# Performance work log

Hardware: AMD Instinct MI355X
Metric: run time of the kernel (lower is better)

The kernel has to match this reference:

```python
import jax, jax.numpy as jnp
import numpy as np

MAX_LENGTH = 41
SOS_index = 0


def setup_inputs() -> dict:
    key = jax.random.key(0)
    ks = jax.random.split(key, 16)
    B, S, H, V = 32, 41, 1024, 16384
    sc = 0.02
    inp = {
        "encoder_outputs": jax.random.normal(ks[0], (B, S, H), jnp.float32),
        "encoder_hidden": jax.random.normal(ks[1], (1, B, H), jnp.float32),
        "target_tensor": jax.random.randint(ks[2], (B, MAX_LENGTH), 0, V, jnp.int64),
        # embedding table
        "emb": jax.random.normal(ks[3], (V, H), jnp.float32) * sc,
        # Bahdanau attention params
        "Wq": jax.random.normal(ks[4], (H, H), jnp.float32) * sc,
        "bq": jnp.zeros((H,), jnp.float32),
        "Wk": jax.random.normal(ks[5], (H, H), jnp.float32) * sc,
        "bk": jnp.zeros((H,), jnp.float32),
        "Vw": jax.random.normal(ks[6], (1, H), jnp.float32) * sc,
        "bV": jnp.zeros((1,), jnp.float32),
        # LSTM params (PyTorch gate order: i, f, g, o)
        "Wih": jax.random.normal(ks[7], (4 * H, 2 * H), jnp.float32) * sc,
        "Whh": jax.random.normal(ks[8], (4 * H, H), jnp.float32) * sc,
        "bih": jnp.zeros((4 * H,), jnp.float32),
        "bhh": jnp.zeros((4 * H,), jnp.float32),
        # output projection
        "Wout": jax.random.normal(ks[9], (V, H), jnp.float32) * sc,
        "bout": jnp.zeros((V,), jnp.float32),
    }
    return inp


def reference(encoder_outputs, encoder_hidden, target_tensor, emb,
              Wq, bq, Wk, bk, Vw, bV, Wih, Whh, bih, bhh, Wout, bout):
    B = encoder_outputs.shape[0]
    H = encoder_outputs.shape[2]
    # keys projection is invariant across decode steps
    keys_proj = jnp.einsum('bsh,gh->bsg', encoder_outputs, Wk) + bk  # [B,S,H]
    # teacher-forced input tokens: SOS then target[:, :-1]
    sos = jnp.full((1, B), SOS_index, dtype=target_tensor.dtype)
    tokens = jnp.concatenate([sos, target_tensor.T[:-1]], axis=0)  # [T,B]

    h0 = encoder_hidden[0]            # [B,H]
    c0 = jnp.zeros_like(h0)

    def step(carry, tok):
        h, c = carry
        x = emb[tok]                                       # [B,H] (dropout: eval mode)
        q = h @ Wq.T + bq                                  # [B,H] query from hidden
        e = jnp.tanh(q[:, None, :] + keys_proj)            # [B,S,H]
        scores = jnp.einsum('bsh,h->bs', e, Vw[0]) + bV[0] # [B,S]
        w = jax.nn.softmax(scores, axis=-1)                # [B,S]
        ctx = jnp.einsum('bs,bsh->bh', w, encoder_outputs) # [B,H]
        xi = jnp.concatenate([x, ctx], axis=-1)            # [B,2H]
        gates = xi @ Wih.T + h @ Whh.T + (bih + bhh)       # [B,4H]
        i_g, f_g, g_g, o_g = jnp.split(gates, 4, axis=-1)
        i_g = jax.nn.sigmoid(i_g)
        f_g = jax.nn.sigmoid(f_g)
        g_g = jnp.tanh(g_g)
        o_g = jax.nn.sigmoid(o_g)
        c_new = f_g * c + i_g * g_g
        h_new = o_g * jnp.tanh(c_new)
        logits = h_new @ Wout.T + bout                     # [B,V]
        return (h_new, c_new), (logits, w)

    (h_f, c_f), (logits, attn) = jax.lax.scan(step, (h0, c0), tokens)
    decoder_outputs = jax.nn.log_softmax(logits.transpose(1, 0, 2), axis=-1)  # [B,T,V]
    attentions = attn.transpose(1, 0, 2)                                       # [B,T,S]
    return decoder_outputs, h_f[None], c_f[None], attentions
```

## Files before the change

### kernel.cpp

```cpp
#include <hip/hip_runtime.h>
#include <hip/hip_bf16.h>
#include <math.h>

#define B 32
#define S 41
#define T 41
#define H 1024
#define V 16384
#define BH (B*H)
#define NBLK 256
#define NTHR 512
#define RPB 20

typedef unsigned int uint;
typedef unsigned short ushort;
typedef __attribute__((ext_vector_type(8))) short bf16x8;
typedef __attribute__((ext_vector_type(4))) float f32x4;
typedef _Float16 h2v __attribute__((ext_vector_type(2)));

__device__ __forceinline__ float fast_sigmoid(float x){ return 1.f/(1.f + __expf(-x)); }
__device__ __forceinline__ float fast_tanh(float x){
  float e = __expf(-2.f*fabsf(x));
  float r = (1.f - e)/(1.f + e);
  return copysignf(r, x);
}
__device__ __forceinline__ ushort f2h(float f){ return __builtin_bit_cast(unsigned short, (_Float16)f); }
__device__ __forceinline__ float h2f(ushort u){ return (float)__builtin_bit_cast(_Float16, u); }
__device__ __forceinline__ h2v bc2(uint u){ return __builtin_bit_cast(h2v, u); }
__device__ __forceinline__ ushort f2bf(float f){
  uint u = __float_as_uint(f);
  u = u + 0x7FFFu + ((u>>16)&1u);
  return (ushort)(u>>16);
}

#if defined(__has_builtin)
#if __has_builtin(__builtin_amdgcn_fdot2)
#define HAS_FDOT2 1
#endif
#endif
__device__ __forceinline__ float dot2(h2v a, h2v b, float c){
#ifdef HAS_FDOT2
  return __builtin_amdgcn_fdot2(a, b, c, false);
#else
  return fmaf((float)a.x, (float)b.x, fmaf((float)a.y, (float)b.y, c));
#endif
}

__device__ __forceinline__ void st_sc_f32(float* p, float v){
  asm volatile("global_store_dword %0, %1, off sc0 sc1" :: "v"(p), "v"(v) : "memory");
}
__device__ __forceinline__ void st_sc_u32(uint* p, uint v){
  asm volatile("global_store_dword %0, %1, off sc0 sc1" :: "v"(p), "v"(v) : "memory");
}

__device__ __forceinline__ float ld_sc_f32(const float* p){
  float r;
  asm volatile("global_load_dword %0, %1, off sc0 sc1\n\ts_waitcnt vmcnt(0)"
               : "=v"(r) : "v"(p) : "memory");
  return r;
}
__device__ __forceinline__ void ldx8_sc(const uint* p, uint4* r){
  asm volatile(
    "global_load_dwordx4 %0, %8, off sc0 sc1\n\t"
    "global_load_dwordx4 %1, %8, off offset:16 sc0 sc1\n\t"
    "global_load_dwordx4 %2, %8, off offset:32 sc0 sc1\n\t"
    "global_load_dwordx4 %3, %8, off offset:48 sc0 sc1\n\t"
    "global_load_dwordx4 %4, %8, off offset:64 sc0 sc1\n\t"
    "global_load_dwordx4 %5, %8, off offset:80 sc0 sc1\n\t"
    "global_load_dwordx4 %6, %8, off offset:96 sc0 sc1\n\t"
    "global_load_dwordx4 %7, %8, off offset:112 sc0 sc1\n\t"
    "s_waitcnt vmcnt(0)"
    : "=&v"(r[0]), "=&v"(r[1]), "=&v"(r[2]), "=&v"(r[3]),
      "=&v"(r[4]), "=&v"(r[5]), "=&v"(r[6]), "=&v"(r[7])
    : "v"(p) : "memory");
}
__device__ __forceinline__ void ld_qgh_sc(const float* qp, const float* gp,
                                          float4* q, float* gh){
  asm volatile(
    "global_load_dwordx4 %0, %5, off sc0 sc1\n\t"
    "global_load_dwordx4 %1, %5, off offset:16 sc0 sc1\n\t"
    "global_load_dwordx4 %2, %5, off offset:32 sc0 sc1\n\t"
    "global_load_dwordx4 %3, %5, off offset:48 sc0 sc1\n\t"
    "global_load_dword  %4, %6, off sc0 sc1\n\t"
    "s_waitcnt vmcnt(0)"
    : "=&v"(q[0]), "=&v"(q[1]), "=&v"(q[2]), "=&v"(q[3]), "=&v"(*gh)
    : "v"(qp), "v"(gp) : "memory");
}

__device__ __forceinline__ void gbar_flat(uint* cnt, uint target){
  asm volatile("s_waitcnt vmcnt(0)" ::: "memory");
  __syncthreads();
  if (threadIdx.x == 0){
    __hip_atomic_fetch_add(cnt, 1u, __ATOMIC_RELAXED, __HIP_MEMORY_SCOPE_AGENT);
    while (__hip_atomic_load(cnt, __ATOMIC_RELAXED, __HIP_MEMORY_SCOPE_AGENT) < target)
      __builtin_amdgcn_s_sleep(1);
  }
  __syncthreads();
}

__global__ __launch_bounds__(256) void k_init(const float* __restrict__ eh,
                                              ushort* __restrict__ h16, uint* __restrict__ bar){
  int i = blockIdx.x*256 + threadIdx.x;
  h16[i] = f2h(eh[i]);
  if (i < 1024) bar[i] = 0;
}

__global__ __launch_bounds__(256) void k_bsum(const float* __restrict__ a,
                                              const float* __restrict__ b, float* __restrict__ o){
  int i = blockIdx.x*256 + threadIdx.x;
  o[i] = a[i] + b[i];
}

__global__ __launch_bounds__(256) void k_gather(const float* __restrict__ emb,
    const int* __restrict__ tgt, float* __restrict__ Xall){
  int r = blockIdx.x;
  int t = r / B, b = r % B;
  int tok = (t==0) ? 0 : tgt[b*T + (t-1)];
  const float4* src = (const float4*)(emb + (size_t)tok*H);
  float4* dst = (float4*)(Xall + (size_t)r*H);
  dst[threadIdx.x] = src[threadIdx.x];
}

__global__ __launch_bounds__(256) void k_cvt16(const float* __restrict__ src,
                                               ushort* __restrict__ dst, int n8){
  int i = blockIdx.x*256 + threadIdx.x;
  if (i >= n8) return;
  const float4* s4 = (const float4*)src + (size_t)i*2;
  float4 a = s4[0], b = s4[1];
  union { ushort us[8]; uint4 v; } p;
  p.us[0]=f2h(a.x); p.us[1]=f2h(a.y); p.us[2]=f2h(a.z); p.us[3]=f2h(a.w);
  p.us[4]=f2h(b.x); p.us[5]=f2h(b.y); p.us[6]=f2h(b.z); p.us[7]=f2h(b.w);
  ((uint4*)dst)[i] = p.v;
}

__global__ __launch_bounds__(256) void k_bgemm(const float* __restrict__ A,
    const float* __restrict__ W, const float* __restrict__ bias, float* __restrict__ C,
    int M, int N, int wstride, int woff)
{
  __shared__ ushort As[128*40];
  __shared__ ushort Bs[128*40];
  const int tid = threadIdx.x;
  const int n0 = blockIdx.x*128, m0 = blockIdx.y*128;
  const int row = tid>>1, half = tid&1;
  const int lane = tid & 63, widx = tid >> 6;
  const int wm = (widx>>1)*64, wn = (widx&1)*64;

  int arow = m0 + row; if (arow > M-1) arow = M-1;
  const float* ga = A + (size_t)arow*1024 + half*16;
  const float* gw = W + (size_t)(n0+row)*wstride + woff + half*16;
  ushort* sa = &As[row*40 + half*16];
  ushort* sb = &Bs[row*40 + half*16];

  f32x4 acc[4][4] = {};

  for (int k0 = 0; k0 < 1024; k0 += 32) {
    float4 a0 = *(const float4*)(ga+k0),   a1 = *(const float4*)(ga+k0+4);
    float4 a2 = *(const float4*)(ga+k0+8), a3 = *(const float4*)(ga+k0+12);
    float4 w0 = *(const float4*)(gw+k0),   w1 = *(const float4*)(gw+k0+4);
    float4 w2 = *(const float4*)(gw+k0+8), w3 = *(const float4*)(gw+k0+12);
    __syncthreads();
    {
      union { ushort us[8]; uint4 v; } p, q;
      p.us[0]=f2bf(a0.x); p.us[1]=f2bf(a0.y); p.us[2]=f2bf(a0.z); p.us[3]=f2bf(a0.w);
      p.us[4]=f2bf(a1.x); p.us[5]=f2bf(a1.y); p.us[6]=f2bf(a1.z); p.us[7]=f2bf(a1.w);
      q.us[0]=f2bf(a2.x); q.us[1]=f2bf(a2.y); q.us[2]=f2bf(a2.z); q.us[3]=f2bf(a2.w);
      q.us[4]=f2bf(a3.x); q.us[5]=f2bf(a3.y); q.us[6]=f2bf(a3.z); q.us[7]=f2bf(a3.w);
      *(uint4*)sa = p.v; *(uint4*)(sa+8) = q.v;
      p.us[0]=f2bf(w0.x); p.us[1]=f2bf(w0.y); p.us[2]=f2bf(w0.z); p.us[3]=f2bf(w0.w);
      p.us[4]=f2bf(w1.x); p.us[5]=f2bf(w1.y); p.us[6]=f2bf(w1.z); p.us[7]=f2bf(w1.w);
      q.us[0]=f2bf(w2.x); q.us[1]=f2bf(w2.y); q.us[2]=f2bf(w2.z); q.us[3]=f2bf(w2.w);
      q.us[4]=f2bf(w3.x); q.us[5]=f2bf(w3.y); q.us[6]=f2bf(w3.z); q.us[7]=f2bf(w3.w);
      *(uint4*)sb = p.v; *(uint4*)(sb+8) = q.v;
    }
    __syncthreads();
    bf16x8 af[4], bf[4];
    #pragma unroll
    for (int i=0;i<4;i++)
      af[i] = *(const bf16x8*)&As[(wm + i*16 + (lane&15))*40 + (lane>>4)*8];
    #pragma unroll
    for (int j=0;j<4;j++)
      bf[j] = *(const bf16x8*)&Bs[(wn + j*16 + (lane&15))*40 + (lane>>4)*8];
    #pragma unroll
    for (int i=0;i<4;i++)
      #pragma unroll
      for (int j=0;j<4;j++)
        acc[i][j] = __builtin_amdgcn_mfma_f32_16x16x32_bf16(af[i], bf[j], acc[i][j], 0, 0, 0);
  }

  #pragma unroll
  for (int i=0;i<4;i++){
    #pragma unroll
    for (int j=0;j<4;j++){
      int n = n0 + wn + j*16 + (lane&15);
      float bv = bias ? bias[n] : 0.f;
      #pragma unroll
      for (int qq=0;qq<4;qq++){
        int m = m0 + wm + i*16 + ((lane>>4)<<2) + qq;
        if (m < M) C[(size_t)m*N + n] = acc[i][j][qq] + bv;
      }
    }
  }
}

__global__ __launch_bounds__(512, 2) void k_loop(
    const ushort* __restrict__ Wc16,
    const float* __restrict__ bq,
    const ushort* __restrict__ keys16,
    const float* __restrict__ Vw, const float* __restrict__ bV,
    const float* __restrict__ GxF,
    const ushort* __restrict__ encW16,
    float* __restrict__ qg,
    float* __restrict__ ghg,
    ushort* __restrict__ h16,
    float* __restrict__ hhist,
    float* __restrict__ attn_out,
    float* __restrict__ hf, float* __restrict__ cf,
    uint* __restrict__ bar,
    float* __restrict__ pscore)
{
  __shared__ __align__(16) uint   w_lds[RPB*516];
  __shared__ __align__(16) ushort ew_lds[512*42];
  __shared__ __align__(16) float  red[RPB*512];
  __shared__ float sc_sh[64];
  __shared__ float ga[512];
  __shared__ float hsh[128];

  const int tid = threadIdx.x;
  const int bid = blockIdx.x;
  const int pb_b = bid >> 3, pb_mc = bid & 7;
  const int lane = tid & 63, wv = tid >> 6;
  uint* h16u = (uint*)h16;

  const int pa_b = tid & 31, pa_ks = tid >> 5;
  const int gn = (tid >> 7)*H + pb_mc*128 + (tid & 127);

  const int na = bid*RPB + (tid>>5);
  const int nb = bid*RPB + 16 + (tid>>5);
  const float bqa = (na < H) ? bq[na] : 0.f;
  const float bqb = (tid < 128 && nb < H) ? bq[nb] : 0.f;

  uint* qcnt = &bar[0];
  uint* hcnt = &bar[16];
  uint* scnt = &bar[256 + pb_b*8];
  const int my_s = pb_mc + 8*wv;

  for (int i = tid; i < RPB*128; i += NTHR){
    int r = i >> 7, j = i & 127;
    uint4 v = *((const uint4*)(Wc16 + (size_t)(bid*RPB + r)*1024) + j);
    *(uint4*)&w_lds[r*516 + j*4] = v;
  }
  for (int s = 0; s < S; ++s)
    ew_lds[tid*42 + s] = encW16[((size_t)pb_b*S + s)*4096 + gn];
  float vreg[16];
  {
    const float4* vp = (const float4*)(Vw + lane*16);
    *(float4*)&vreg[0] = vp[0]; *(float4*)&vreg[4]  = vp[1];
    *(float4*)&vreg[8] = vp[2]; *(float4*)&vreg[12] = vp[3];
  }
  const float bV0 = bV[0];
  float creg = 0.f;
  __syncthreads();

  for (int t = 0; t < T; ++t) {
    float gxv;
    {
      uint4 hr[8];
      ldx8_sc((const uint*)h16u + pa_b*512 + pa_ks*32, hr);
      float part[RPB];
      #pragma unroll
      for (int r = 0; r < RPB; ++r){
        const uint* wr = &w_lds[r*516 + pa_ks*32];
        float a0 = 0.f, a1 = 0.f;
        #pragma unroll
        for (int j = 0; j < 8; ++j){
          uint4 w = *(const uint4*)(wr + j*4);
          uint4 h = hr[j];
          a0 = dot2(bc2(w.x), bc2(h.x), a0);
          a1 = dot2(bc2(w.y), bc2(h.y), a1);
          a0 = dot2(bc2(w.z), bc2(h.z), a0);
          a1 = dot2(bc2(w.w), bc2(h.w), a1);
        }
        part[r] = a0 + a1;
      }
      #pragma unroll
      for (int r = 0; r < RPB; ++r) red[r*512 + pa_ks*32 + pa_b] = part[r];
      __syncthreads();
      {
        int r = tid >> 5, b2 = tid & 31;
        const float* rp = &red[r*512 + b2];
        float s = 0.f;
        #pragma unroll
        for (int k2 = 0; k2 < 16; ++k2) s += rp[k2*32];
        if (na < H) st_sc_f32(&qg[b2*H + na], s + bqa);
        else        st_sc_f32(&ghg[(size_t)b2*4*H + (na - H)], s);
      }
      if (tid < 128){
        int r = 16 + (tid >> 5), b2 = tid & 31;
        const float* rp = &red[r*512 + b2];
        float s = 0.f;
        #pragma unroll
        for (int k2 = 0; k2 < 16; ++k2) s += rp[k2*32];
        if (nb < H) st_sc_f32(&qg[b2*H + nb], s + bqb);
        else        st_sc_f32(&ghg[(size_t)b2*4*H + (nb - H)], s);
      }
      gxv = GxF[((size_t)t*B + pb_b)*4*H + gn];
    }
    gbar_flat(qcnt, 256u*(uint)(t+1));

    {
      float4 q4[4]; float ghv;
      ld_qgh_sc(qg + pb_b*H + lane*16, ghg + (size_t)pb_b*4*H + gn, q4, &ghv);
      float qarr[16];
      *(float4*)&qarr[0] = q4[0]; *(float4*)&qarr[4]  = q4[1];
      *(float4*)&qarr[8] = q4[2]; *(float4*)&qarr[12] = q4[3];

      if (my_s < S) {
        const ushort* kr = keys16 + ((size_t)pb_b*S + my_s)*H + lane*16;
        uint4 k0 = *(const uint4*)kr;
        uint4 k1 = *(const uint4*)(kr + 8);
        float part = 0.f;
        #define SC2(u, e) { h2v hh = bc2(u); \
          part += fast_tanh(qarr[e]   + (float)hh.x) * vreg[e]; \
          part += fast_tanh(qarr[e+1] + (float)hh.y) * vreg[e+1]; }
        SC2(k0.x,0) SC2(k0.y,2) SC2(k0.z,4) SC2(k0.w,6)
        SC2(k1.x,8) SC2(k1.y,10) SC2(k1.z,12) SC2(k1.w,14)
        #undef SC2
        #pragma unroll
        for (int off = 32; off > 0; off >>= 1) part += __shfl_xor(part, off);
        if (lane == 0) st_sc_f32(&pscore[pb_b*64 + my_s], part + bV0);
      }
      asm volatile("s_waitcnt vmcnt(0)" ::: "memory");
      __syncthreads();
      if (tid == 0){
        __hip_atomic_fetch_add(scnt, 1u, __ATOMIC_RELAXED, __HIP_MEMORY_SCOPE_AGENT);
        while (__hip_atomic_load(scnt, __ATOMIC_RELAXED, __HIP_MEMORY_SCOPE_AGENT) < 8u*(uint)(t+1))
          __builtin_amdgcn_s_sleep(1);
      }
      __syncthreads();
      if (tid < 64) {
        float val = (tid < S) ? ld_sc_f32(&pscore[pb_b*64 + tid]) : -1e30f;
        float m = val;
        #pragma unroll
        for (int off = 32; off > 0; off >>= 1) m = fmaxf(m, __shfl_xor(m, off));
        float e = (tid < S) ? __expf(val - m) : 0.f;
        float ssum = e;
        #pragma unroll
        for (int off = 32; off > 0; off >>= 1) ssum += __shfl_xor(ssum, off);
        if (tid < S) {
          float w = e / ssum;
          sc_sh[tid] = w;
          if (pb_mc == 0) attn_out[((size_t)pb_b*T + t)*S + tid] = w;
        }
      }
      __syncthreads();
      {
        float acc = gxv + ghv;
        const ushort* ep = &ew_lds[tid*42];
        #pragma unroll
        for (int s = 0; s < S; ++s)
          acc = fmaf(sc_sh[s], h2f(ep[s]), acc);
        ga[tid] = acc;
      }
      __syncthreads();
      if (tid < 128) {
        float ig = fast_sigmoid(ga[tid]);
        float fg = fast_sigmoid(ga[128+tid]);
        float gg = fast_tanh   (ga[256+tid]);
        float og = fast_sigmoid(ga[384+tid]);
        creg = fg*creg + ig*gg;
        float hn = og * fast_tanh(creg);
        int m = pb_mc*128 + tid;
        hsh[tid] = hn;
        __builtin_nontemporal_store(hn, &hhist[((size_t)pb_b*T + t)*H + m]);
        if (t == T-1) { hf[pb_b*H + m] = hn; cf[pb_b*H + m] = creg; }
      }
      __syncthreads();
      if (tid < 64) {
        uint pk = (uint)f2h(hsh[2*tid]) | ((uint)f2h(hsh[2*tid+1]) << 16);
        st_sc_u32(&h16u[(size_t)pb_b*512 + pb_mc*64 + tid], pk);
      }
    }
    if (t < T-1) gbar_flat(hcnt, 256u*(uint)(t+1));
  }
}

__global__ __launch_bounds__(256) void k_logsm(float* __restrict__ p_all)
{
  float* p = p_all + (size_t)blockIdx.x * V;
  const int tid = threadIdx.x;
  const int lane = tid & 63, wave = tid >> 6;
  __shared__ float red[4];
  float4 v[16];
  float m = -1e30f;
  #pragma unroll
  for (int j=0;j<16;j++){
    v[j] = *(const float4*)(p + 4*(tid + 256*j));
    m = fmaxf(m, fmaxf(fmaxf(v[j].x, v[j].y), fmaxf(v[j].z, v[j].w)));
  }
  #pragma unroll
  for (int off=32; off>0; off>>=1) m = fmaxf(m, __shfl_xor(m, off));
  if (lane==0) red[wave] = m;
  __syncthreads();
  m = fmaxf(fmaxf(red[0], red[1]), fmaxf(red[2], red[3]));
  float ssum = 0.f;
  #pragma unroll
  for (int j=0;j<16;j++){
    ssum += __expf(v[j].x - m) + __expf(v[j].y - m) + __expf(v[j].z - m) + __expf(v[j].w - m);
  }
  #pragma unroll
  for (int off=32; off>0; off>>=1) ssum += __shfl_xor(ssum, off);
  __syncthreads();
  if (lane==0) red[wave] = ssum;
  __syncthreads();
  float lse = m + __logf(red[0] + red[1] + red[2] + red[3]);
  #pragma unroll
  for (int j=0;j<16;j++){
    float4 o; o.x = v[j].x - lse; o.y = v[j].y - lse; o.z = v[j].z - lse; o.w = v[j].w - lse;
    *(float4*)(p + 4*(tid + 256*j)) = o;
  }
}

extern "C" void kernel_launch(void* const* d_in, const int* in_sizes, int n_in,
                              void* d_out, int out_size, void* d_ws, size_t ws_size,
                              hipStream_t stream) {
  const float* enc   = (const float*)d_in[0];
  const float* ehid  = (const float*)d_in[1];
  const int*   tgt   = (const int*)  d_in[2];
  const float* emb   = (const float*)d_in[3];
  const float* Wq    = (const float*)d_in[4];
  const float* bq    = (const float*)d_in[5];
  const float* Wk    = (const float*)d_in[6];
  const float* bk    = (const float*)d_in[7];
  const float* Vw    = (const float*)d_in[8];
  const float* bV    = (const float*)d_in[9];
  const float* Wih   = (const float*)d_in[10];
  const float* Whh   = (const float*)d_in[11];
  const float* bih   = (const float*)d_in[12];
  const float* bhh   = (const float*)d_in[13];
  const float* Wout  = (const float*)d_in[14];
  const float* bout  = (const float*)d_in[15];

  float* out  = (float*)d_out;
  float* dec  = out;
  float* hf   = out + (size_t)B*T*V;
  float* cf   = hf + BH;
  float* attn = cf + BH;

  float*  Xall   = dec;
  float*  keysF  = dec +  1343488;
  float*  GxF    = dec +  2686976;
  float*  encWF  = dec +  8060928;
  ushort* keys16 = (ushort*)(dec + 13434880);
  ushort* encW16 = (ushort*)(dec + 14106624);
  ushort* Wc16   = (ushort*)(dec + 16793600);

  float* ws = (float*)d_ws;
  float*  hhist = ws;
  float*  bsum  = ws + 1343488;
  ushort* h16   = (ushort*)(ws + 1347584);
  float*  qg    = ws + 1363968;
  float*  ghg   = ws + 1396736;
  uint*   bar   = (uint*)(ws + 1527808);
  float*  pscore= ws + 1528832;

  k_init<<<BH/256, 256, 0, stream>>>(ehid, h16, bar);
  k_bsum<<<(4*H)/256, 256, 0, stream>>>(bih, bhh, bsum);
  k_gather<<<T*B, 256, 0, stream>>>(emb, tgt, Xall);

  { dim3 g(H/128, 11);     k_bgemm<<<g, 256, 0, stream>>>(enc,  Wk,  bk,     keysF, B*S, H,   H,   0); }
  { dim3 g((4*H)/128, 11); k_bgemm<<<g, 256, 0, stream>>>(Xall, Wih, bsum,   GxF,   T*B, 4*H, 2*H, 0); }
  { dim3 g((4*H)/128, 11); k_bgemm<<<g, 256, 0, stream>>>(enc,  Wih, nullptr,encWF, B*S, 4*H, 2*H, H); }

  k_cvt16<<<(B*S*H/8 + 255)/256, 256, 0, stream>>>(keysF, keys16, B*S*H/8);
  k_cvt16<<<(B*S*4*H/8 + 255)/256, 256, 0, stream>>>(encWF, encW16, B*S*4*H/8);
  k_cvt16<<<(H*H/8 + 255)/256, 256, 0, stream>>>(Wq,  Wc16,             H*H/8);
  k_cvt16<<<(4*H*H/8 + 255)/256, 256, 0, stream>>>(Whh, Wc16 + (size_t)H*H, 4*H*H/8);

  {
    void* kargs[] = {
      (void*)&Wc16, (void*)&bq, (void*)&keys16, (void*)&Vw, (void*)&bV,
      (void*)&GxF, (void*)&encW16, (void*)&qg, (void*)&ghg,
      (void*)&h16, (void*)&hhist, (void*)&attn, (void*)&hf, (void*)&cf,
      (void*)&bar, (void*)&pscore
    };
    hipLaunchCooperativeKernel((const void*)k_loop, dim3(NBLK), dim3(NTHR), kargs, 0, stream);
  }

  { dim3 g(V/128, 11);     k_bgemm<<<g, 256, 0, stream>>>(hhist, Wout, bout, dec, B*T, V, H, 0); }
  k_logsm<<<B*T, 256, 0, stream>>>(dec);
}
```

Measured before the change: 1.568 ms.

## Replace atomic grid barriers with per-block flags and local score computation

Removes the atomic-counter grid barriers and uses per-block epoch flags instead. After the query phase, each block publishes a flag and waits until all 256 flags reach the step. Before the hidden-state matvec, each block waits only on the 8 producer blocks whose h slices it reads. Each block now computes all 41 attention scores itself into LDS, which removes the per-batch sub-barrier and the global pscore exchange at the cost of redundant score work across the 8 blocks that share a batch. The aim is lower synchronisation latency per step. The trade-off is more polling traffic and relaxed-ordering correctness that depends on the sc0/sc1 stores and the waitcnt.

Result: faster. 1.531 ms (-2.4%).

```diff
diff --git a/kernel.cpp b/kernel.cpp
--- a/kernel.cpp
+++ b/kernel.cpp
@@ -53,9 +53,15 @@
   asm volatile("global_store_dword %0, %1, off sc0 sc1" :: "v"(p), "v"(v) : "memory");
 }
 
-__device__ __forceinline__ float ld_sc_f32(const float* p){
-  float r;
+__device__ __forceinline__ uint ld_sc_u32(const uint* p){
+  uint r;
   asm volatile("global_load_dword %0, %1, off sc0 sc1\n\ts_waitcnt vmcnt(0)"
+               : "=v"(r) : "v"(p) : "memory");
+  return r;
+}
+__device__ __forceinline__ uint4 ld_sc_u128(const uint4* p){
+  uint4 r;
+  asm volatile("global_load_dwordx4 %0, %1, off sc0 sc1\n\ts_waitcnt vmcnt(0)"
                : "=v"(r) : "v"(p) : "memory");
   return r;
 }
@@ -85,17 +91,6 @@
     "s_waitcnt vmcnt(0)"
     : "=&v"(q[0]), "=&v"(q[1]), "=&v"(q[2]), "=&v"(q[3]), "=&v"(*gh)
     : "v"(qp), "v"(gp) : "memory");
-}
-
-__device__ __forceinline__ void gbar_flat(uint* cnt, uint target){
-  asm volatile("s_waitcnt vmcnt(0)" ::: "memory");
-  __syncthreads();
-  if (threadIdx.x == 0){
-    __hip_atomic_fetch_add(cnt, 1u, __ATOMIC_RELAXED, __HIP_MEMORY_SCOPE_AGENT);
-    while (__hip_atomic_load(cnt, __ATOMIC_RELAXED, __HIP_MEMORY_SCOPE_AGENT) < target)
-      __builtin_amdgcn_s_sleep(1);
-  }
-  __syncthreads();
 }
 
 __global__ __launch_bounds__(256) void k_init(const float* __restrict__ eh,
@@ -215,8 +210,7 @@
     float* __restrict__ hhist,
     float* __restrict__ attn_out,
     float* __restrict__ hf, float* __restrict__ cf,
-    uint* __restrict__ bar,
-    float* __restrict__ pscore)
+    uint* __restrict__ bar)
 {
   __shared__ __align__(16) uint   w_lds[RPB*516];
   __shared__ __align__(16) ushort ew_lds[512*42];
@@ -231,6 +225,9 @@
   const int lane = tid & 63, wv = tid >> 6;
   uint* h16u = (uint*)h16;
 
+  uint* paf = bar;
+  uint* hfl = bar + 256;
+
   const int pa_b = tid & 31, pa_ks = tid >> 5;
   const int gn = (tid >> 7)*H + pb_mc*128 + (tid & 127);
 
@@ -238,11 +235,6 @@
   const int nb = bid*RPB + 16 + (tid>>5);
   const float bqa = (na < H) ? bq[na] : 0.f;
   const float bqb = (tid < 128 && nb < H) ? bq[nb] : 0.f;
-
-  uint* qcnt = &bar[0];
-  uint* hcnt = &bar[16];
-  uint* scnt = &bar[256 + pb_b*8];
-  const int my_s = pb_mc + 8*wv;
 
   for (int i = tid; i < RPB*128; i += NTHR){
     int r = i >> 7, j = i & 127;
@@ -264,6 +256,15 @@
   for (int t = 0; t < T; ++t) {
     float gxv;
     {
+      if (t > 0){
+        const uint* fp = &hfl[pa_b*8 + (pa_ks>>1)];
+        const uint tgt = (uint)t;
+        while (true){
+          uint f = ld_sc_u32(fp);
+          if (__all(f >= tgt)) break;
+          __builtin_amdgcn_s_sleep(1);
+        }
+      }
       uint4 hr[8];
       ldx8_sc((const uint*)h16u + pa_b*512 + pa_ks*32, hr);
       float part[RPB];
@@ -305,7 +306,19 @@
       }
       gxv = GxF[((size_t)t*B + pb_b)*4*H + gn];
     }
-    gbar_flat(qcnt, 256u*(uint)(t+1));
+    asm volatile("s_waitcnt vmcnt(0)" ::: "memory");
+    __syncthreads();
+    if (tid < 64){
+      if (tid == 0) st_sc_u32(&paf[bid], (uint)(t+1));
+      const uint tgt = (uint)(t+1);
+      while (true){
+        uint4 f = ld_sc_u128((const uint4*)paf + tid);
+        bool ok = (f.x >= tgt) & (f.y >= tgt) & (f.z >= tgt) & (f.w >= tgt);
+        if (__all(ok)) break;
+        __builtin_amdgcn_s_sleep(1);
+      }
+    }
+    __syncthreads();
 
     {
       float4 q4[4]; float ghv;
@@ -314,8 +327,8 @@
       *(float4*)&qarr[0] = q4[0]; *(float4*)&qarr[4]  = q4[1];
       *(float4*)&qarr[8] = q4[2]; *(float4*)&qarr[12] = q4[3];
 
-      if (my_s < S) {
-        const ushort* kr = keys16 + ((size_t)pb_b*S + my_s)*H + lane*16;
+      for (int s = wv; s < S; s += 8) {
+        const ushort* kr = keys16 + ((size_t)pb_b*S + s)*H + lane*16;
         uint4 k0 = *(const uint4*)kr;
         uint4 k1 = *(const uint4*)(kr + 8);
         float part = 0.f;
@@ -327,18 +340,11 @@
         #undef SC2
         #pragma unroll
         for (int off = 32; off > 0; off >>= 1) part += __shfl_xor(part, off);
-        if (lane == 0) st_sc_f32(&pscore[pb_b*64 + my_s], part + bV0);
-      }
-      asm volatile("s_waitcnt vmcnt(0)" ::: "memory");
-      __syncthreads();
-      if (tid == 0){
-        __hip_atomic_fetch_add(scnt, 1u, __ATOMIC_RELAXED, __HIP_MEMORY_SCOPE_AGENT);
-        while (__hip_atomic_load(scnt, __ATOMIC_RELAXED, __HIP_MEMORY_SCOPE_AGENT) < 8u*(uint)(t+1))
-          __builtin_amdgcn_s_sleep(1);
+        if (lane == 0) sc_sh[s] = part + bV0;
       }
       __syncthreads();
       if (tid < 64) {
-        float val = (tid < S) ? ld_sc_f32(&pscore[pb_b*64 + tid]) : -1e30f;
+        float val = (tid < S) ? sc_sh[tid] : -1e30f;
         float m = val;
         #pragma unroll
         for (int off = 32; off > 0; off >>= 1) m = fmaxf(m, __shfl_xor(m, off));
@@ -375,12 +381,13 @@
         if (t == T-1) { hf[pb_b*H + m] = hn; cf[pb_b*H + m] = creg; }
       }
       __syncthreads();
-      if (tid < 64) {
+      if (t < T-1 && tid < 64) {
         uint pk = (uint)f2h(hsh[2*tid]) | ((uint)f2h(hsh[2*tid+1]) << 16);
         st_sc_u32(&h16u[(size_t)pb_b*512 + pb_mc*64 + tid], pk);
+        asm volatile("s_waitcnt vmcnt(0)" ::: "memory");
+        if (tid == 0) st_sc_u32(&hfl[bid], (uint)(t+1));
       }
     }
-    if (t < T-1) gbar_flat(hcnt, 256u*(uint)(t+1));
   }
 }
 
@@ -461,7 +468,6 @@
   float*  qg    = ws + 1363968;
   float*  ghg   = ws + 1396736;
   uint*   bar   = (uint*)(ws + 1527808);
-  float*  pscore= ws + 1528832;
 
   k_init<<<BH/256, 256, 0, stream>>>(ehid, h16, bar);
   k_bsum<<<(4*H)/256, 256, 0, stream>>>(bih, bhh, bsum);
@@ -480,8 +486,7 @@
     void* kargs[] = {
       (void*)&Wc16, (void*)&bq, (void*)&keys16, (void*)&Vw, (void*)&bV,
       (void*)&GxF, (void*)&encW16, (void*)&qg, (void*)&ghg,
-      (void*)&h16, (void*)&hhist, (void*)&attn, (void*)&hf, (void*)&cf,
-      (void*)&bar, (void*)&pscore
+      (void*)&h16, (void*)&hhist, (void*)&attn, (void*)&hf, (void*)&cf, (void*)&bar
     };
     hipLaunchCooperativeKernel((const void*)k_loop, dim3(NBLK), dim3(NTHR), kargs, 0, stream);
   }
```
